# Kernel optimization log

Hardware: AMD Instinct MI355X
Metric: run time of the kernel (lower is better)

The kernel has to match this reference:

```python
import jax, jax.numpy as jnp
import numpy as np

R_BLOCKS = 64
BLOCK_SIZE = 64
N_ELEMENTS = BLOCK_SIZE * (BLOCK_SIZE - 1) // 2  # 2016
NUM_NEUMANN_TERMS = 5

# strict upper-triangle indices (constants)
_TRIU_ROWS, _TRIU_COLS = np.triu_indices(BLOCK_SIZE, k=1)


def skew_symmetric(vec):
    # vec: (r, n_elements) -> (r, block, block) skew-symmetric
    r = vec.shape[0]
    m = jnp.zeros((r, BLOCK_SIZE, BLOCK_SIZE), dtype=vec.dtype)
    m = m.at[:, _TRIU_ROWS, _TRIU_COLS].set(vec)
    return m - jnp.swapaxes(m, -2, -1)


def cayley_neumann(weight):
    # R = I + 2Q + 2Q^2 + ... (truncated Neumann series of (I+Q)(I-Q)^-1)
    Q = skew_symmetric(weight)                     # (r, b, b)
    I = jnp.eye(BLOCK_SIZE, dtype=weight.dtype)
    R = jnp.broadcast_to(I, Q.shape) + 2.0 * Q
    Q_sq = jnp.matmul(Q, Q)
    R = R + 2.0 * Q_sq
    Q_pow = Q_sq
    for _ in range(3, NUM_NEUMANN_TERMS):
        Q_pow = jnp.matmul(Q_pow, Q)
        R = R + 2.0 * Q_pow
    return R


def setup_inputs() -> dict:
    key = jax.random.key(0)
    k1, k2 = jax.random.split(key)
    x = jax.random.normal(k1, (4, 4096, R_BLOCKS * BLOCK_SIZE), dtype=jnp.float32)
    weight = jax.random.normal(k2, (R_BLOCKS, N_ELEMENTS), dtype=jnp.float32) * 0.02
    return {"x": x, "weight": weight}


def reference(x, weight):
    rot = cayley_neumann(weight)                   # (r, block, block)
    B, S, D = x.shape
    x_r = x.reshape(B, S, R_BLOCKS, BLOCK_SIZE)    # (B, S, r, k)
    y = jnp.einsum('bsrk,rkc->bsrc', x_r, rot)
    return y.reshape(B, S, D)
```

## Files before the change

### kernel.cpp

```cpp
#include <hip/hip_runtime.h>
#include <hip/hip_bf16.h>

typedef __bf16 bf16x8 __attribute__((ext_vector_type(8)));
typedef float  f32x4  __attribute__((ext_vector_type(4)));

#define BS 64
#define RB 64
#define NELEM 2016
#define DD 4096
#define MROWS 16384
#define TILES 8

__global__ __launch_bounds__(256) void rot_kernel(const float* __restrict__ w,
                                                  __bf16* __restrict__ Rpk) {
    const int bid   = blockIdx.x;
    const int blk   = bid >> 2;
    const int rbase = (bid & 3) * 16;
    const int t     = threadIdx.x;
    __shared__ float Q [BS * BS];
    __shared__ float T0[16 * BS];
    __shared__ float T1[16 * BS];
    const float* wb = w + blk * NELEM;

    for (int e = t; e < BS * BS; e += 256) {
        const int i = e >> 6, j = e & 63;
        float v = 0.f;
        if (i < j)      v =  wb[63 * i - (i * (i - 1)) / 2 + (j - i - 1)];
        else if (i > j) v = -wb[63 * j - (j * (j - 1)) / 2 + (i - j - 1)];
        Q[e] = v;
    }
    __syncthreads();

    const int j  = t & 63;
    const int s4 = (t >> 6) * 4;

    float qcol[BS];
#pragma unroll
    for (int k = 0; k < BS; ++k) qcol[k] = Q[k * BS + j];

    float racc[4];
#pragma unroll
    for (int s = 0; s < 4; ++s) {
        const int i = rbase + s4 + s;
        racc[s] = (i == j ? 1.f : 0.f) + 2.f * Q[i * BS + j];
    }

#pragma unroll
    for (int s = 0; s < 4; ++s) {
        const int i = rbase + s4 + s;
        float sum = 0.f;
#pragma unroll
        for (int k = 0; k < BS; ++k) sum += Q[i * BS + k] * qcol[k];
        T0[(s4 + s) * BS + j] = sum;
        racc[s] += 2.f * sum;
    }
    __syncthreads();

#pragma unroll
    for (int s = 0; s < 4; ++s) {
        const int r = s4 + s;
        float sum = 0.f;
#pragma unroll
        for (int k = 0; k < BS; ++k) sum += T0[r * BS + k] * qcol[k];
        T1[r * BS + j] = sum;
        racc[s] += 2.f * sum;
    }
    __syncthreads();

#pragma unroll
    for (int s = 0; s < 4; ++s) {
        const int r = s4 + s;
        float sum = 0.f;
#pragma unroll
        for (int k = 0; k < BS; ++k) sum += T1[r * BS + k] * qcol[k];
        racc[s] += 2.f * sum;
    }

#pragma unroll
    for (int s = 0; s < 4; ++s) {
        const int i  = rbase + s4 + s;
        const int kf = i >> 5;
        const int g  = (i >> 3) & 3;
        const int jj = i & 7;
        const int lane = 16 * g + (j & 15);
        const int n    = j >> 4;
        Rpk[(size_t)((blk * 8 + kf * 4 + n) * 64 + lane) * 8 + jj] = (__bf16)racc[s];
    }
}

__global__ __launch_bounds__(256) void apply_kernel(const float* __restrict__ x,
                                                    const __bf16* __restrict__ Rpk,
                                                    float* __restrict__ y) {
    const int tid  = threadIdx.x;
    const int l    = tid & 63;
    const int W    = blockIdx.x * 4 + (tid >> 6);
    const int rblk = W & 63;
    const int rg   = W >> 6;
    const int g    = l >> 4;
    const int c    = l & 15;

    bf16x8 bfrag[2][4];
    const bf16x8* rp = reinterpret_cast<const bf16x8*>(Rpk) + (size_t)rblk * 8 * 64 + l;
#pragma unroll
    for (int kf = 0; kf < 2; ++kf)
#pragma unroll
        for (int n = 0; n < 4; ++n)
            bfrag[kf][n] = rp[(kf * 4 + n) * 64];

    const long rowbase = (long)rg * (TILES * 16);
    const float* xlane = x + (rowbase + (l & 15)) * (long)DD + rblk * 64 + g * 8;

    const f32x4 zero = {0.f, 0.f, 0.f, 0.f};

    f32x4 v[4], vn[4];
#pragma unroll
    for (int q = 0; q < 4; ++q)
        v[q] = *reinterpret_cast<const f32x4*>(xlane + (q >> 1) * 32 + (q & 1) * 4);

#pragma unroll
    for (int t = 0; t < TILES; ++t) {
        if (t + 1 < TILES) {
            const float* xp = xlane + (long)(t + 1) * 16 * DD;
#pragma unroll
            for (int q = 0; q < 4; ++q)
                vn[q] = *reinterpret_cast<const f32x4*>(xp + (q >> 1) * 32 + (q & 1) * 4);
        }

        bf16x8 a0, a1;
#pragma unroll
        for (int e = 0; e < 4; ++e) {
            a0[e]     = (__bf16)v[0][e];
            a0[e + 4] = (__bf16)v[1][e];
            a1[e]     = (__bf16)v[2][e];
            a1[e + 4] = (__bf16)v[3][e];
        }

        f32x4 acc[4];
#pragma unroll
        for (int n = 0; n < 4; ++n)
            acc[n] = __builtin_amdgcn_mfma_f32_16x16x32_bf16(a0, bfrag[0][n], zero, 0, 0, 0);
#pragma unroll
        for (int n = 0; n < 4; ++n)
            acc[n] = __builtin_amdgcn_mfma_f32_16x16x32_bf16(a1, bfrag[1][n], acc[n], 0, 0, 0);

        float* yl = y + (rowbase + t * 16 + 4 * g) * (long)DD + rblk * 64 + c;
#pragma unroll
        for (int n = 0; n < 4; ++n)
#pragma unroll
            for (int i = 0; i < 4; ++i)
                __builtin_nontemporal_store(acc[n][i], yl + (long)i * DD + n * 16);

        if (t + 1 < TILES) {
#pragma unroll
            for (int q = 0; q < 4; ++q) v[q] = vn[q];
        }
    }
}

extern "C" void kernel_launch(void* const* d_in, const int* in_sizes, int n_in,
                              void* d_out, int out_size, void* d_ws, size_t ws_size,
                              hipStream_t stream) {
    (void)in_sizes; (void)n_in; (void)out_size; (void)ws_size;
    const float* x = (const float*)d_in[0];
    const float* w = (const float*)d_in[1];
    float* y = (float*)d_out;
    __bf16* Rpk = (__bf16*)d_ws;

    rot_kernel<<<RB * 4, 256, 0, stream>>>(w, Rpk);

    const int waves  = RB * (MROWS / (TILES * 16));
    const int blocks = waves / 4;
    apply_kernel<<<blocks, 256, 0, stream>>>(x, Rpk, y);
}
```

Baseline: 117.9 us.

## Stage x tiles through LDS with direct global-to-LDS async loads

```diff
diff --git a/kernel.cpp b/kernel.cpp
--- a/kernel.cpp
+++ b/kernel.cpp
@@ -91,9 +91,11 @@
 __global__ __launch_bounds__(256) void apply_kernel(const float* __restrict__ x,
                                                     const __bf16* __restrict__ Rpk,
                                                     float* __restrict__ y) {
+    __shared__ float xs[4][1024];
     const int tid  = threadIdx.x;
     const int l    = tid & 63;
-    const int W    = blockIdx.x * 4 + (tid >> 6);
+    const int wv   = tid >> 6;
+    const int W    = blockIdx.x * 4 + wv;
     const int rblk = W & 63;
     const int rg   = W >> 6;
     const int g    = l >> 4;
@@ -108,33 +110,51 @@
             bfrag[kf][n] = rp[(kf * 4 + n) * 64];
 
     const long rowbase = (long)rg * (TILES * 16);
-    const float* xlane = x + (rowbase + (l & 15)) * (long)DD + rblk * 64 + g * 8;
 
-    const f32x4 zero = {0.f, 0.f, 0.f, 0.f};
+    const float* srcq[4];
+#pragma unroll
+    for (int q = 0; q < 4; ++q) {
+        const int srow = 4 * q + (l >> 4);
+        const int schk = (l & 15) ^ srow;
+        srcq[q] = x + (rowbase + srow) * (long)DD + rblk * 64 + schk * 4;
+    }
+    float* const ldsb = &xs[wv][0];
 
-    f32x4 v[4], vn[4];
-#pragma unroll
-    for (int q = 0; q < 4; ++q)
-        v[q] = *reinterpret_cast<const f32x4*>(xlane + (q >> 1) * 32 + (q & 1) * 4);
+#define STAGE(tt) do {                                                         \
+    const long roff_ = (long)(tt) * 16 * DD;                                   \
+    _Pragma("unroll")                                                          \
+    for (int q_ = 0; q_ < 4; ++q_)                                             \
+        __builtin_amdgcn_global_load_lds(                                      \
+            (const __attribute__((address_space(1))) void*)(srcq[q_] + roff_), \
+            (__attribute__((address_space(3))) void*)(ldsb + q_ * 256),        \
+            16, 0, 0);                                                         \
+} while (0)
+
+    STAGE(0);
+    asm volatile("s_waitcnt vmcnt(0)" ::: "memory");
+    __builtin_amdgcn_sched_barrier(0);
 
 #pragma unroll
     for (int t = 0; t < TILES; ++t) {
-        if (t + 1 < TILES) {
-            const float* xp = xlane + (long)(t + 1) * 16 * DD;
-#pragma unroll
-            for (int q = 0; q < 4; ++q)
-                vn[q] = *reinterpret_cast<const f32x4*>(xp + (q >> 1) * 32 + (q & 1) * 4);
-        }
+        f32x4 v0 = *reinterpret_cast<const f32x4*>(&xs[wv][c * 64 + (((2 * g + 0) ^ c) << 2)]);
+        f32x4 v1 = *reinterpret_cast<const f32x4*>(&xs[wv][c * 64 + (((2 * g + 1) ^ c) << 2)]);
+        f32x4 v2 = *reinterpret_cast<const f32x4*>(&xs[wv][c * 64 + (((8 + 2 * g + 0) ^ c) << 2)]);
+        f32x4 v3 = *reinterpret_cast<const f32x4*>(&xs[wv][c * 64 + (((8 + 2 * g + 1) ^ c) << 2)]);
 
         bf16x8 a0, a1;
 #pragma unroll
         for (int e = 0; e < 4; ++e) {
-            a0[e]     = (__bf16)v[0][e];
-            a0[e + 4] = (__bf16)v[1][e];
-            a1[e]     = (__bf16)v[2][e];
-            a1[e + 4] = (__bf16)v[3][e];
+            a0[e]     = (__bf16)v0[e];
+            a0[e + 4] = (__bf16)v1[e];
+            a1[e]     = (__bf16)v2[e];
+            a1[e + 4] = (__bf16)v3[e];
         }
 
+        asm volatile("s_waitcnt lgkmcnt(0)" ::: "memory");
+        __builtin_amdgcn_sched_barrier(0);
+        if (t + 1 < TILES) STAGE(t + 1);
+
+        const f32x4 zero = {0.f, 0.f, 0.f, 0.f};
         f32x4 acc[4];
 #pragma unroll
         for (int n = 0; n < 4; ++n)
@@ -150,11 +170,10 @@
             for (int i = 0; i < 4; ++i)
                 __builtin_nontemporal_store(acc[n][i], yl + (long)i * DD + n * 16);
 
-        if (t + 1 < TILES) {
-#pragma unroll
-            for (int q = 0; q < 4; ++q) v[q] = vn[q];
-        }
+        asm volatile("s_waitcnt vmcnt(16)" ::: "memory");
+        __builtin_amdgcn_sched_barrier(0);
     }
+#undef STAGE
 }
 
 extern "C" void kernel_launch(void* const* d_in, const int* in_sizes, int n_in,
```

After: 120.8 us. +2.5%, slower.

## Remap apply waves to row-tile × column-quarter, streaming rotation blocks per step

Applied to the files above, without the earlier changes.

```diff
diff --git a/kernel.cpp b/kernel.cpp
--- a/kernel.cpp
+++ b/kernel.cpp
@@ -9,7 +9,6 @@
 #define NELEM 2016
 #define DD 4096
 #define MROWS 16384
-#define TILES 8
 
 __global__ __launch_bounds__(256) void rot_kernel(const float* __restrict__ w,
                                                   __bf16* __restrict__ Rpk) {
@@ -93,22 +92,20 @@
                                                     float* __restrict__ y) {
     const int tid  = threadIdx.x;
     const int l    = tid & 63;
-    const int W    = blockIdx.x * 4 + (tid >> 6);
-    const int rblk = W & 63;
-    const int rg   = W >> 6;
+    const int wv   = tid >> 6;
+    const int W    = blockIdx.x * 4 + wv;
+    const int qd   = W & 3;
+    const int rg   = W >> 2;
     const int g    = l >> 4;
     const int c    = l & 15;
 
-    bf16x8 bfrag[2][4];
-    const bf16x8* rp = reinterpret_cast<const bf16x8*>(Rpk) + (size_t)rblk * 8 * 64 + l;
-#pragma unroll
-    for (int kf = 0; kf < 2; ++kf)
-#pragma unroll
-        for (int n = 0; n < 4; ++n)
-            bfrag[kf][n] = rp[(kf * 4 + n) * 64];
+    const long rowbase = (long)rg * 16;
+    const long colbase = qd * 1024;
 
-    const long rowbase = (long)rg * (TILES * 16);
-    const float* xlane = x + (rowbase + (l & 15)) * (long)DD + rblk * 64 + g * 8;
+    const float* xlane = x + (rowbase + (l & 15)) * (long)DD + colbase + g * 8;
+
+    const bf16x8* rp = reinterpret_cast<const bf16x8*>(Rpk)
+                     + ((size_t)(qd * 16) * 8) * 64 + l;
 
     const f32x4 zero = {0.f, 0.f, 0.f, 0.f};
 
@@ -117,13 +114,26 @@
     for (int q = 0; q < 4; ++q)
         v[q] = *reinterpret_cast<const f32x4*>(xlane + (q >> 1) * 32 + (q & 1) * 4);
 
+    bf16x8 bfc[2][4], bfn[2][4];
 #pragma unroll
-    for (int t = 0; t < TILES; ++t) {
-        if (t + 1 < TILES) {
-            const float* xp = xlane + (long)(t + 1) * 16 * DD;
+    for (int kf = 0; kf < 2; ++kf)
+#pragma unroll
+        for (int n = 0; n < 4; ++n)
+            bfc[kf][n] = rp[(kf * 4 + n) * 64];
+
+#pragma unroll
+    for (int rr = 0; rr < 16; ++rr) {
+        if (rr + 1 < 16) {
+            const float* xp = xlane + (rr + 1) * 64;
 #pragma unroll
             for (int q = 0; q < 4; ++q)
                 vn[q] = *reinterpret_cast<const f32x4*>(xp + (q >> 1) * 32 + (q & 1) * 4);
+            const bf16x8* rpn = rp + (size_t)(rr + 1) * 512;
+#pragma unroll
+            for (int kf = 0; kf < 2; ++kf)
+#pragma unroll
+                for (int n = 0; n < 4; ++n)
+                    bfn[kf][n] = rpn[(kf * 4 + n) * 64];
         }
 
         bf16x8 a0, a1;
@@ -138,21 +148,26 @@
         f32x4 acc[4];
 #pragma unroll
         for (int n = 0; n < 4; ++n)
-            acc[n] = __builtin_amdgcn_mfma_f32_16x16x32_bf16(a0, bfrag[0][n], zero, 0, 0, 0);
+            acc[n] = __builtin_amdgcn_mfma_f32_16x16x32_bf16(a0, bfc[0][n], zero, 0, 0, 0);
 #pragma unroll
         for (int n = 0; n < 4; ++n)
-            acc[n] = __builtin_amdgcn_mfma_f32_16x16x32_bf16(a1, bfrag[1][n], acc[n], 0, 0, 0);
+            acc[n] = __builtin_amdgcn_mfma_f32_16x16x32_bf16(a1, bfc[1][n], acc[n], 0, 0, 0);
 
-        float* yl = y + (rowbase + t * 16 + 4 * g) * (long)DD + rblk * 64 + c;
+        float* yl = y + (rowbase + 4 * g) * (long)DD + colbase + rr * 64 + c;
 #pragma unroll
         for (int n = 0; n < 4; ++n)
 #pragma unroll
             for (int i = 0; i < 4; ++i)
                 __builtin_nontemporal_store(acc[n][i], yl + (long)i * DD + n * 16);
 
-        if (t + 1 < TILES) {
+        if (rr + 1 < 16) {
 #pragma unroll
             for (int q = 0; q < 4; ++q) v[q] = vn[q];
+#pragma unroll
+            for (int kf = 0; kf < 2; ++kf)
+#pragma unroll
+                for (int n = 0; n < 4; ++n)
+                    bfc[kf][n] = bfn[kf][n];
         }
     }
 }
@@ -168,7 +183,7 @@
 
     rot_kernel<<<RB * 4, 256, 0, stream>>>(w, Rpk);
 
-    const int waves  = RB * (MROWS / (TILES * 16));
+    const int waves  = (MROWS / 16) * 4;
     const int blocks = waves / 4;
     apply_kernel<<<blocks, 256, 0, stream>>>(x, Rpk, y);
 }
```

New measurement: 162.0 us. 37.4% more time.
